# Kernel optimization log

Hardware: AMD Instinct MI355X
Metric: run time of the kernel (lower is better)

Reference implementation:

```python
import jax, jax.numpy as jnp
import numpy as np
import math

B, L, D_MODEL, D_K, H = 2, 1024, 1024, 1024, 16
HD = D_K // H  # 64, even
EPS = 1e-5


def setup_inputs() -> dict:
    key = jax.random.key(0)
    ks = jax.random.split(key, 16)
    s = 0.02
    inp = {
        'word_embed': jax.random.normal(ks[0], (B, L, D_MODEL), jnp.float32),
        'speaker_embed': jax.random.normal(ks[1], (B, L, D_MODEL), jnp.float32),
        'mask': jnp.broadcast_to(jnp.tril(jnp.ones((L, L), jnp.int32)), (B, L, L)),
        'qw_w': jax.random.normal(ks[2], (D_K, D_MODEL), jnp.float32) * s,
        'qw_b': jnp.zeros((D_K,), jnp.float32),
        'kw_w': jax.random.normal(ks[3], (D_K, D_MODEL), jnp.float32) * s,
        'kw_b': jnp.zeros((D_K,), jnp.float32),
        'qs_w': jax.random.normal(ks[4], (D_K, D_MODEL), jnp.float32) * s,
        'qs_b': jnp.zeros((D_K,), jnp.float32),
        'ks_w': jax.random.normal(ks[5], (D_K, D_MODEL), jnp.float32) * s,
        'ks_b': jnp.zeros((D_K,), jnp.float32),
        'v_w': jax.random.normal(ks[6], (D_K, D_MODEL), jnp.float32) * s,
        'v_b': jnp.zeros((D_K,), jnp.float32),
        'out_w': jax.random.normal(ks[7], (D_MODEL, D_K), jnp.float32) * s,
        'out_b': jnp.zeros((D_MODEL,), jnp.float32),
        'gamma': jnp.ones((HD,), jnp.float32),
        'beta': jnp.zeros((HD,), jnp.float32),
    }
    return inp


def _rotary_tables(seq_len, dim, dtype):
    pos = jnp.arange(seq_len, dtype=dtype)[:, None]  # [L,1]
    div = jnp.exp(jnp.arange(0, dim, 2, dtype=dtype) * (-math.log(10000.0) / dim))
    return jnp.sin(pos * div), jnp.cos(pos * div)  # each [L, dim//2]


def _rotary(x, sin, cos):
    # x: [B,H,L,HD]; NOTE: original concatenates halves (non-interleaved output)
    x1, x2 = x[..., 0::2], x[..., 1::2]
    return jnp.concatenate([x1 * cos - x2 * sin, x1 * sin + x2 * cos], axis=-1)


def _layernorm(x, gamma, beta):
    mu = jnp.mean(x, axis=-1, keepdims=True)
    var = jnp.mean(jnp.square(x - mu), axis=-1, keepdims=True)
    return (x - mu) * jax.lax.rsqrt(var + EPS) * gamma + beta


def _split(x):
    b, l, _ = x.shape
    return x.reshape(b, l, H, HD).transpose(0, 2, 1, 3)  # [B,H,L,HD]


def reference(word_embed, speaker_embed, mask, qw_w, qw_b, kw_w, kw_b,
              qs_w, qs_b, ks_w, ks_b, v_w, v_b, out_w, out_b, gamma, beta):
    proj = lambda x, w, b: jnp.einsum('bld,kd->blk', x, w) + b
    qw = _split(proj(word_embed, qw_w, qw_b))
    kw = _split(proj(word_embed, kw_w, kw_b))
    qs = _split(proj(speaker_embed, qs_w, qs_b))
    ks = _split(proj(speaker_embed, ks_w, ks_b))
    v = _split(proj(word_embed, v_w, v_b))

    sin, cos = _rotary_tables(word_embed.shape[1], HD, word_embed.dtype)
    ln = lambda x: _layernorm(_rotary(x, sin, cos), gamma, beta)
    qw, kw, qs, ks = ln(qw), ln(kw), ln(qs), ln(ks)

    scores = (jnp.einsum('bhqd,bhkd->bhqk', qw, kw)
              + jnp.einsum('bhqd,bhkd->bhqk', qs, ks)) / math.sqrt(2 * HD)
    scores = jnp.where(mask[:, None] == 0, -jnp.inf, scores)
    attn = jax.nn.softmax(scores, axis=-1)  # dropout is eval-mode no-op
    out = jnp.einsum('bhqk,bhkd->bhqd', attn, v)
    out = out.transpose(0, 2, 1, 3).reshape(out.shape[0], out.shape[2], D_K)
    out = jnp.einsum('blk,dk->bld', out, out_w) + out_b
    return (out, attn)
```

## Files before the change

kernel.cpp:

```cpp
#include <hip/hip_runtime.h>
#include <cstdint>
#include <cstddef>

typedef __bf16 bf16x8 __attribute__((ext_vector_type(8)));
typedef float  f32x4  __attribute__((ext_vector_type(4)));
typedef unsigned short ushort8_t __attribute__((ext_vector_type(8)));

__device__ __forceinline__ unsigned short f2bf(float f){
  unsigned u = __builtin_bit_cast(unsigned, f);
  u += 0x7fffu + ((u >> 16) & 1u);
  return (unsigned short)(u >> 16);
}
__device__ __forceinline__ float bf2f(unsigned short s){
  return __builtin_bit_cast(float, ((unsigned)s) << 16);
}

#define MFMA16(a,b,c) __builtin_amdgcn_mfma_f32_16x16x32_bf16((a),(b),(c),0,0,0)

__device__ __forceinline__ void gload16(const void* g, void* lds){
  __builtin_amdgcn_global_load_lds(
      (const __attribute__((address_space(1))) void*)g,
      (__attribute__((address_space(3))) void*)lds, 16, 0, 0);
}

#define E_XW    ((size_t)0)
#define E_XS    (E_XW    + (size_t)2048*1024)
#define E_WWORD (E_XS    + (size_t)2048*1024)
#define E_WSPK  (E_WWORD + (size_t)3072*1024)
#define E_WOUT  (E_WSPK  + (size_t)2048*1024)
#define E_PWORD (E_WOUT  + (size_t)1024*1024)
#define E_PSPK  (E_PWORD + (size_t)2048*3072)
#define E_VT    (E_PSPK  + (size_t)2048*2048)
#define E_CTX   (E_VT    + (size_t)2048*1024)
#define E_END   (E_CTX   + (size_t)2048*1024)

__global__ __launch_bounds__(256) void convert_all(
    const float* __restrict__ word, const float* __restrict__ spk,
    const float* __restrict__ qww,  const float* __restrict__ kww,
    const float* __restrict__ vw,   const float* __restrict__ qsw,
    const float* __restrict__ ksw,  const float* __restrict__ outw,
    const float* __restrict__ qwb,  const float* __restrict__ kwb,
    const float* __restrict__ vb,   const float* __restrict__ qsb,
    const float* __restrict__ ksb,
    unsigned short* __restrict__ wsb, float* __restrict__ FB)
{
  int idx = blockIdx.x*256 + threadIdx.x;
  if (idx < 32768){
    int pos = idx >> 5, i = idx & 31;
    float inv = expf((float)(2*i) * -0.14391157f);
    float ang = (float)pos * inv;
    float sv, cv; sincosf(ang, &sv, &cv);
    FB[5120 + idx]         = sv;
    FB[5120 + 32768 + idx] = cv;
  } else if (idx < 33792){
    int i = idx - 32768;
    FB[i] = qwb[i]; FB[1024+i] = kwb[i]; FB[2048+i] = vb[i];
    FB[3072+i] = qsb[i]; FB[3072+1024+i] = ksb[i];
  }

  const size_t total = 2621440;
  for (size_t c = (size_t)blockIdx.x*256 + threadIdx.x; c < total;
       c += (size_t)gridDim.x*256){
    const float* src; size_t dst; size_t i;
    if (c < 524288)       { src = word; dst = E_XW; i = c; }
    else if (c < 1048576) { src = spk;  dst = E_XS; i = c - 524288; }
    else {
      size_t t = c - 1048576; int seg = (int)(t >> 18); i = t & 262143;
      switch (seg){
        case 0:  src = qww; dst = E_WWORD;                      break;
        case 1:  src = kww; dst = E_WWORD + (size_t)1048576;    break;
        case 2:  src = vw;  dst = E_WWORD + (size_t)2097152;    break;
        case 3:  src = qsw; dst = E_WSPK;                       break;
        case 4:  src = ksw; dst = E_WSPK  + (size_t)1048576;    break;
        default: src = outw; dst = E_WOUT;                      break;
      }
    }
    float4 v = ((const float4*)src)[i];
    ushort4 o; o.x = f2bf(v.x); o.y = f2bf(v.y); o.z = f2bf(v.z); o.w = f2bf(v.w);
    ((ushort4*)(wsb + dst))[i] = o;
  }
}

template<int NF>
__device__ __forceinline__ void gemm_body(
    const unsigned short* __restrict__ A, const unsigned short* __restrict__ Bw,
    const float* __restrict__ bias, void* __restrict__ Cv,
    int N, int bid, int out_bf16,
    unsigned short* As, unsigned short* Bs)
{
  const int K = 1024;
  const int BN = NF*32;
  const int nbn = N / BN;
  const int bm = bid / nbn, bn = bid % nbn;
  const int tid = threadIdx.x;
  const int l = tid & 63, w = tid >> 6;
  const int wm = w >> 1, wn = w & 1;
  const int li = l & 15, lg = l >> 4;

  f32x4 acc[4][NF];
  #pragma unroll
  for (int a = 0; a < 4; a++)
    #pragma unroll
    for (int b = 0; b < NF; b++) acc[a][b] = (f32x4){0.f,0.f,0.f,0.f};

  const int colS = (l & 3) * 8;
  const size_t aBase = (size_t)(bm*128) * K;
  const size_t bBase = (size_t)(bn*BN) * K;

  for (int kt = 0; kt < K; kt += 32){
    #pragma unroll
    for (int j = 0; j < 2; j++){
      int row = (w*2 + j)*16 + (l >> 2);
      gload16(A + aBase + (size_t)row*K + kt + colS, &As[(size_t)(w*2+j)*512]);
    }
    if (NF == 4){
      #pragma unroll
      for (int j = 0; j < 2; j++){
        int row = (w*2 + j)*16 + (l >> 2);
        gload16(Bw + bBase + (size_t)row*K + kt + colS, &Bs[(size_t)(w*2+j)*512]);
      }
    } else {
      int row = w*16 + (l >> 2);
      gload16(Bw + bBase + (size_t)row*K + kt + colS, &Bs[(size_t)w*512]);
    }
    asm volatile("s_waitcnt vmcnt(0)" ::: "memory");
    __syncthreads();

    bf16x8 af[4], bfr[NF];
    const int ko = lg * 8;
    #pragma unroll
    for (int fm = 0; fm < 4; fm++)
      af[fm] = *(const bf16x8*)&As[(wm*64 + fm*16 + li)*32 + ko];
    #pragma unroll
    for (int fn = 0; fn < NF; fn++)
      bfr[fn] = *(const bf16x8*)&Bs[(wn*(NF*16) + fn*16 + li)*32 + ko];
    #pragma unroll
    for (int fm = 0; fm < 4; fm++)
      #pragma unroll
      for (int fn = 0; fn < NF; fn++)
        acc[fm][fn] = MFMA16(af[fm], bfr[fn], acc[fm][fn]);
    __syncthreads();
  }

  #pragma unroll
  for (int fm = 0; fm < 4; fm++){
    int m0 = bm*128 + wm*64 + fm*16 + lg*4;
    #pragma unroll
    for (int fn = 0; fn < NF; fn++){
      int n = bn*BN + wn*(NF*16) + fn*16 + li;
      float bv = bias[n];
      #pragma unroll
      for (int r = 0; r < 4; r++){
        float v = acc[fm][fn][r] + bv;
        if (out_bf16) ((unsigned short*)Cv)[(size_t)(m0+r)*N + n] = f2bf(v);
        else          ((float*)Cv)[(size_t)(m0+r)*N + n] = v;
      }
    }
  }
}

__global__ __launch_bounds__(256) void gemm_qkv(
    const unsigned short* __restrict__ XW, const unsigned short* __restrict__ WWORD,
    const unsigned short* __restrict__ XS, const unsigned short* __restrict__ WSPK,
    const float* __restrict__ FB,
    unsigned short* __restrict__ PWORD, unsigned short* __restrict__ PSPK)
{
  __shared__ unsigned short As[128*32];
  __shared__ unsigned short Bs[128*32];
  int raw = blockIdx.x;
  int bid = (raw & 7)*80 + (raw >> 3);
  if (bid < 384)
    gemm_body<4>(XW, WWORD, FB,        PWORD, 3072, bid,       1, As, Bs);
  else
    gemm_body<4>(XS, WSPK,  FB + 3072, PSPK,  2048, bid - 384, 1, As, Bs);
}

__global__ __launch_bounds__(256) void gemm_out(
    const unsigned short* __restrict__ CTX, const unsigned short* __restrict__ WOUT,
    const float* __restrict__ outb, float* __restrict__ outp)
{
  __shared__ unsigned short As[128*32];
  __shared__ unsigned short Bs[64*32];
  int raw = blockIdx.x;
  int bid = (raw & 7)*32 + (raw >> 3);
  gemm_body<2>(CTX, WOUT, outb, outp, 1024, bid, 0, As, Bs);
}

__global__ __launch_bounds__(256) void postproc(
    unsigned short* __restrict__ Pw, unsigned short* __restrict__ Ps,
    const float* __restrict__ gamma, const float* __restrict__ beta,
    const float* __restrict__ TS, const float* __restrict__ TC,
    unsigned short* __restrict__ VT)
{
  __shared__ float lds[2320];
  int bx = blockIdx.x;
  int t = threadIdx.x;
  if (bx < 4096){
    int sec = bx & 3, rp = bx >> 2;
    int half = t >> 7, c = t & 127;
    int row = rp*2 + half;
    int seg = c >> 3, j = c & 7;
    unsigned short* p;
    if      (sec == 0) p = Pw + (size_t)row*3072 +        seg*64;
    else if (sec == 1) p = Pw + (size_t)row*3072 + 1024 + seg*64;
    else if (sec == 2) p = Ps + (size_t)row*2048 +        seg*64;
    else               p = Ps + (size_t)row*2048 + 1024 + seg*64;
    int pos = row & 1023;
    int sl  = half*16 + seg;

    ushort8_t xv = *(const ushort8_t*)(p + j*8);
    float4 sv = *(const float4*)&TS[pos*32 + j*4];
    float4 cv = *(const float4*)&TC[pos*32 + j*4];
    float ss[4] = {sv.x, sv.y, sv.z, sv.w};
    float cc[4] = {cv.x, cv.y, cv.z, cv.w};
    float y1[4], y2[4];
    #pragma unroll
    for (int k = 0; k < 4; k++){
      float x0 = bf2f(xv[2*k]), x1 = bf2f(xv[2*k+1]);
      y1[k] = x0*cc[k] - x1*ss[k];
      y2[k] = x0*ss[k] + x1*cc[k];
    }
    *(float4*)&lds[sl*68 + j*4]      = (float4){y1[0], y1[1], y1[2], y1[3]};
    *(float4*)&lds[sl*68 + 32 + j*4] = (float4){y2[0], y2[1], y2[2], y2[3]};
    __syncthreads();

    float4 a0 = *(const float4*)&lds[sl*68 + j*8];
    float4 a1 = *(const float4*)&lds[sl*68 + j*8 + 4];
    float v[8] = {a0.x, a0.y, a0.z, a0.w, a1.x, a1.y, a1.z, a1.w};
    float s = 0.f;
    #pragma unroll
    for (int k = 0; k < 8; k++) s += v[k];
    #pragma unroll
    for (int o = 1; o < 8; o <<= 1) s += __shfl_xor(s, o);
    float mu = s * (1.f/64.f);
    float sq = 0.f;
    #pragma unroll
    for (int k = 0; k < 8; k++){ float d = v[k] - mu; sq += d*d; }
    #pragma unroll
    for (int o = 1; o < 8; o <<= 1) sq += __shfl_xor(sq, o);
    float rs = rsqrtf(sq * (1.f/64.f) + 1e-5f);
    float4 g0 = *(const float4*)&gamma[j*8], g1 = *(const float4*)&gamma[j*8+4];
    float4 b0 = *(const float4*)&beta[j*8],  b1 = *(const float4*)&beta[j*8+4];
    float gg[8] = {g0.x,g0.y,g0.z,g0.w,g1.x,g1.y,g1.z,g1.w};
    float bb[8] = {b0.x,b0.y,b0.z,b0.w,b1.x,b1.y,b1.z,b1.w};
    ushort8_t o8;
    #pragma unroll
    for (int k = 0; k < 8; k++) o8[k] = f2bf((v[k]-mu)*rs*gg[k] + bb[k]);
    *(ushort8_t*)(p + j*8) = o8;
  } else {
    unsigned short* tp = (unsigned short*)lds;
    int bid2 = bx - 4096;
    int bh = bid2 >> 4, lt = bid2 & 15;
    int b = bh >> 4, h = bh & 15;
    #pragma unroll
    for (int i = 0; i < 2; i++){
      int cc2 = t + i*256;
      int row = cc2 >> 3, co = (cc2 & 7)*8;
      const unsigned short* src = Pw + (size_t)(b*1024 + lt*64 + row)*3072 + 2048 + h*64 + co;
      *(uint4*)&tp[row*72 + co] = *(const uint4*)src;
    }
    __syncthreads();
    int d = t >> 2, jb = (t & 3)*16;
    unsigned short o[16];
    #pragma unroll
    for (int j = 0; j < 16; j++) o[j] = tp[(jb + j)*72 + d];
    unsigned short* dst = VT + ((size_t)bh*64 + d)*1024 + lt*64 + jb;
    *(uint4*)dst       = *(uint4*)&o[0];
    *(uint4*)(dst + 8) = *(uint4*)&o[8];
  }
}

__global__ __launch_bounds__(512) void attn_fused(
    const unsigned short* __restrict__ Pw, const unsigned short* __restrict__ Ps,
    const unsigned short* __restrict__ VTg,
    float* __restrict__ attn, unsigned short* __restrict__ Ctx)
{
  __shared__ unsigned short SL[36864];

  int bx = blockIdx.x;
  int b = bx >> 7, rem = bx & 127, h = rem >> 3, qq = rem & 7;
  int maxkt = 15 - qq;
  int tid = threadIdx.x;
  int w = tid >> 6, l = tid & 63;
  int g = w >> 2, wsub = w & 3;
  int qt = g ? maxkt : qq;
  int lg = l >> 4, li = l & 15;
  int q0 = qt*64 + wsub*16;
  int bh = b*16 + h;

  int srow = tid >> 3, scb = tid & 7;
  const unsigned short* gKW = Pw + (size_t)(b*1024)*3072 + 1024 + h*64;
  const unsigned short* gKS = Ps + (size_t)(b*1024)*2048 + 1024 + h*64;
  const unsigned short* gVT = VTg + (size_t)bh*64*1024;
  unsigned short* pt = SL + 27648 + w*1152;

  bf16x8 aqw[2], aqs[2];
  {
    int q = q0 + li;
    const unsigned short* pqw = Pw + (size_t)(b*1024 + q)*3072 + h*64 + lg*8;
    const unsigned short* pqs = Ps + (size_t)(b*1024 + q)*2048 + h*64 + lg*8;
    aqw[0] = *(const bf16x8*)pqw;  aqw[1] = *(const bf16x8*)(pqw + 32);
    aqs[0] = *(const bf16x8*)pqs;  aqs[1] = *(const bf16x8*)(pqs + 32);
  }
  const float rscale = 0.08838834764831845f;

  uint4 rkw, rks, rvt;

  float ps4[4] = {0.f, 0.f, 0.f, 0.f};
  rkw = *(const uint4*)(gKW + (size_t)srow*3072 + scb*8);
  rks = *(const uint4*)(gKS + (size_t)srow*2048 + scb*8);
  *(uint4*)(SL +        srow*72 + scb*8) = rkw;
  *(uint4*)(SL + 9216 + srow*72 + scb*8) = rks;

  for (int kt = 0; kt <= maxkt; ++kt){
    int buf = kt & 1;
    if (kt < maxkt){
      rkw = *(const uint4*)(gKW + (size_t)((kt+1)*64 + srow)*3072 + scb*8);
      rks = *(const uint4*)(gKS + (size_t)((kt+1)*64 + srow)*2048 + scb*8);
    }
    __syncthreads();
    if (kt <= qt){
      const unsigned short* KWt = SL +        buf*4608;
      const unsigned short* KSt = SL + 9216 + buf*4608;
      f32x4 s[4];
      #pragma unroll
      for (int fn = 0; fn < 4; fn++){
        s[fn] = (f32x4){0.f,0.f,0.f,0.f};
        int rr = (fn*16 + li)*72;
        bf16x8 k0 = *(const bf16x8*)(KWt + rr + lg*8);
        bf16x8 k1 = *(const bf16x8*)(KWt + rr + 32 + lg*8);
        bf16x8 k2 = *(const bf16x8*)(KSt + rr + lg*8);
        bf16x8 k3 = *(const bf16x8*)(KSt + rr + 32 + lg*8);
        s[fn] = MFMA16(aqw[0], k0, s[fn]);
        s[fn] = MFMA16(aqw[1], k1, s[fn]);
        s[fn] = MFMA16(aqs[0], k2, s[fn]);
        s[fn] = MFMA16(aqs[1], k3, s[fn]);
      }
      #pragma unroll
      for (int r = 0; r < 4; r++){
        int q = q0 + lg*4 + r;
        #pragma unroll
        for (int fn = 0; fn < 4; fn++){
          int k = kt*64 + fn*16 + li;
          float e = __expf(s[fn][r] * rscale);
          ps4[r] += (k <= q) ? e : 0.f;
        }
      }
    }
    if (kt < maxkt){
      int nb = buf ^ 1;
      *(uint4*)(SL +        nb*4608 + srow*72 + scb*8) = rkw;
      *(uint4*)(SL + 9216 + nb*4608 + srow*72 + scb*8) = rks;
    }
  }
  #pragma unroll
  for (int r = 0; r < 4; r++){
    #pragma unroll
    for (int o = 1; o < 16; o <<= 1) ps4[r] += __shfl_xor(ps4[r], o);
  }
  float rinv[4];
  #pragma unroll
  for (int r = 0; r < 4; r++) rinv[r] = 1.f / ps4[r];

  __syncthreads();
  rkw = *(const uint4*)(gKW + (size_t)srow*3072 + scb*8);
  rks = *(const uint4*)(gKS + (size_t)srow*2048 + scb*8);
  rvt = *(const uint4*)(gVT + (size_t)srow*1024 + scb*8);
  *(uint4*)(SL +         srow*72 + scb*8) = rkw;
  *(uint4*)(SL +  9216 + srow*72 + scb*8) = rks;
  *(uint4*)(SL + 18432 + srow*72 + scb*8) = rvt;

  f32x4 c[4];
  #pragma unroll
  for (int fn = 0; fn < 4; fn++) c[fn] = (f32x4){0.f,0.f,0.f,0.f};

  for (int kt = 0; kt < 16; ++kt){
    int buf = kt & 1;
    if (kt < maxkt){
      rkw = *(const uint4*)(gKW + (size_t)((kt+1)*64 + srow)*3072 + scb*8);
      rks = *(const uint4*)(gKS + (size_t)((kt+1)*64 + srow)*2048 + scb*8);
      rvt = *(const uint4*)(gVT + (size_t)srow*1024 + (kt+1)*64 + scb*8);
    }
    __syncthreads();
    float* abase = attn + ((size_t)bh*1024 + q0 + li)*1024 + kt*64;
    if (kt <= qt){
      const unsigned short* KWt = SL +         buf*4608;
      const unsigned short* KSt = SL +  9216 + buf*4608;
      const unsigned short* VTt = SL + 18432 + buf*4608;
      f32x4 s[4];
      #pragma unroll
      for (int fn = 0; fn < 4; fn++){
        s[fn] = (f32x4){0.f,0.f,0.f,0.f};
        int rr = (fn*16 + li)*72;
        bf16x8 k0 = *(const bf16x8*)(KWt + rr + lg*8);
        bf16x8 k1 = *(const bf16x8*)(KWt + rr + 32 + lg*8);
        bf16x8 k2 = *(const bf16x8*)(KSt + rr + lg*8);
        bf16x8 k3 = *(const bf16x8*)(KSt + rr + 32 + lg*8);
        s[fn] = MFMA16(aqw[0], k0, s[fn]);
        s[fn] = MFMA16(aqw[1], k1, s[fn]);
        s[fn] = MFMA16(aqs[0], k2, s[fn]);
        s[fn] = MFMA16(aqs[1], k3, s[fn]);
      }
      #pragma unroll
      for (int fn = 0; fn < 4; fn++){
        #pragma unroll
        for (int r = 0; r < 4; r++){
          int k = kt*64 + fn*16 + li;
          int q = q0 + lg*4 + r;
          float pp = (k <= q) ? __expf(s[fn][r] * rscale) * rinv[r] : 0.f;
          pt[(lg*4 + r)*72 + fn*16 + li] = f2bf(pp);
        }
      }
      asm volatile("s_waitcnt lgkmcnt(0)" ::: "memory");
      __builtin_amdgcn_sched_barrier(0);
      bf16x8 af0 = *(const bf16x8*)(pt + li*72 + lg*8);
      bf16x8 af1 = *(const bf16x8*)(pt + li*72 + 32 + lg*8);
      ushort8_t u0 = __builtin_bit_cast(ushort8_t, af0);
      ushort8_t u1 = __builtin_bit_cast(ushort8_t, af1);
      *(float4*)(abase + lg*8)          = (float4){bf2f(u0[0]),bf2f(u0[1]),bf2f(u0[2]),bf2f(u0[3])};
      *(float4*)(abase + lg*8 + 4)      = (float4){bf2f(u0[4]),bf2f(u0[5]),bf2f(u0[6]),bf2f(u0[7])};
      *(float4*)(abase + 32 + lg*8)     = (float4){bf2f(u1[0]),bf2f(u1[1]),bf2f(u1[2]),bf2f(u1[3])};
      *(float4*)(abase + 32 + lg*8 + 4) = (float4){bf2f(u1[4]),bf2f(u1[5]),bf2f(u1[6]),bf2f(u1[7])};
      #pragma unroll
      for (int fn = 0; fn < 4; fn++){
        int rr = (fn*16 + li)*72;
        bf16x8 v0 = *(const bf16x8*)(VTt + rr + lg*8);
        bf16x8 v1 = *(const bf16x8*)(VTt + rr + 32 + lg*8);
        c[fn] = MFMA16(af0, v0, c[fn]);
        c[fn] = MFMA16(af1, v1, c[fn]);
      }
    } else {
      float4 z = {0.f, 0.f, 0.f, 0.f};
      *(float4*)(abase + lg*8)          = z;
      *(float4*)(abase + lg*8 + 4)      = z;
      *(float4*)(abase + 32 + lg*8)     = z;
      *(float4*)(abase + 32 + lg*8 + 4) = z;
    }
    if (kt < maxkt){
      int nb = buf ^ 1;
      *(uint4*)(SL +         nb*4608 + srow*72 + scb*8) = rkw;
      *(uint4*)(SL +  9216 + nb*4608 + srow*72 + scb*8) = rks;
      *(uint4*)(SL + 18432 + nb*4608 + srow*72 + scb*8) = rvt;
    }
  }

  #pragma unroll
  for (int fn = 0; fn < 4; fn++){
    #pragma unroll
    for (int r = 0; r < 4; r++){
      int q = q0 + lg*4 + r;
      int d = fn*16 + li;
      Ctx[(size_t)(b*1024 + q)*1024 + h*64 + d] = f2bf(c[fn][r]);
    }
  }
}

extern "C" void kernel_launch(void* const* d_in, const int* in_sizes, int n_in,
                              void* d_out, int out_size, void* d_ws, size_t ws_size,
                              hipStream_t stream)
{
  (void)in_sizes; (void)n_in; (void)out_size; (void)ws_size;
  const float* word = (const float*)d_in[0];
  const float* spk  = (const float*)d_in[1];
  const float* qww  = (const float*)d_in[3];
  const float* qwb  = (const float*)d_in[4];
  const float* kww  = (const float*)d_in[5];
  const float* kwb  = (const float*)d_in[6];
  const float* qsw  = (const float*)d_in[7];
  const float* qsb  = (const float*)d_in[8];
  const float* ksw  = (const float*)d_in[9];
  const float* ksb  = (const float*)d_in[10];
  const float* vw   = (const float*)d_in[11];
  const float* vb   = (const float*)d_in[12];
  const float* outw = (const float*)d_in[13];
  const float* outb = (const float*)d_in[14];
  const float* gamma= (const float*)d_in[15];
  const float* beta = (const float*)d_in[16];

  unsigned short* U = (unsigned short*)d_ws;
  unsigned short* XW    = U + E_XW;
  unsigned short* XS    = U + E_XS;
  unsigned short* WWORD = U + E_WWORD;
  unsigned short* WSPK  = U + E_WSPK;
  unsigned short* WOUT  = U + E_WOUT;
  unsigned short* PWORD = U + E_PWORD;
  unsigned short* PSPK  = U + E_PSPK;
  unsigned short* VT    = U + E_VT;
  unsigned short* CTX   = U + E_CTX;
  float* FB = (float*)(U + E_END);
  float* TS = FB + 5120;
  float* TC = TS + 32768;

  float* outp = (float*)d_out;
  float* attn = outp + (size_t)2*1024*1024;

  convert_all<<<4096, 256, 0, stream>>>(word, spk, qww, kww, vw, qsw, ksw, outw,
                                        qwb, kwb, vb, qsb, ksb, U, FB);
  gemm_qkv<<<640, 256, 0, stream>>>(XW, WWORD, XS, WSPK, FB, PWORD, PSPK);
  postproc<<<4608, 256, 0, stream>>>(PWORD, PSPK, gamma, beta, TS, TC, VT);
  attn_fused<<<256, 512, 0, stream>>>(PWORD, PSPK, VT, attn, CTX);
  gemm_out<<<256, 256, 0, stream>>>(CTX, WOUT, outb, outp);
}
```

Before: 117.8 us.

## Split paired-tile attention blocks into one query tile per block with swizzled order

```diff
diff --git a/kernel.cpp b/kernel.cpp
--- a/kernel.cpp
+++ b/kernel.cpp
@@ -270,25 +270,24 @@
   }
 }
 
-__global__ __launch_bounds__(512) void attn_fused(
+__global__ __launch_bounds__(256) void attn_fused(
     const unsigned short* __restrict__ Pw, const unsigned short* __restrict__ Ps,
     const unsigned short* __restrict__ VTg,
     float* __restrict__ attn, unsigned short* __restrict__ Ctx)
 {
-  __shared__ unsigned short SL[36864];
-
-  int bx = blockIdx.x;
-  int b = bx >> 7, rem = bx & 127, h = rem >> 3, qq = rem & 7;
-  int maxkt = 15 - qq;
+  __shared__ unsigned short SL[32256];
+
+  int raw = blockIdx.x;
+  int bx  = (raw & 7)*64 + (raw >> 3);
+  int b = bx >> 8, rem = bx & 255, h = rem >> 4;
+  int qt = 15 - (rem & 15);
   int tid = threadIdx.x;
   int w = tid >> 6, l = tid & 63;
-  int g = w >> 2, wsub = w & 3;
-  int qt = g ? maxkt : qq;
   int lg = l >> 4, li = l & 15;
-  int q0 = qt*64 + wsub*16;
+  int q0 = qt*64 + w*16;
   int bh = b*16 + h;
 
-  int srow = tid >> 3, scb = tid & 7;
+  int sr = tid >> 3, sc = tid & 7;
   const unsigned short* gKW = Pw + (size_t)(b*1024)*3072 + 1024 + h*64;
   const unsigned short* gKS = Ps + (size_t)(b*1024)*2048 + 1024 + h*64;
   const unsigned short* gVT = VTg + (size_t)bh*64*1024;
@@ -304,23 +303,29 @@
   }
   const float rscale = 0.08838834764831845f;
 
-  uint4 rkw, rks, rvt;
+  uint4 ka0, ka1, kb0, kb1, va0, va1;
 
   float ps4[4] = {0.f, 0.f, 0.f, 0.f};
-  rkw = *(const uint4*)(gKW + (size_t)srow*3072 + scb*8);
-  rks = *(const uint4*)(gKS + (size_t)srow*2048 + scb*8);
-  *(uint4*)(SL +        srow*72 + scb*8) = rkw;
-  *(uint4*)(SL + 9216 + srow*72 + scb*8) = rks;
-
-  for (int kt = 0; kt <= maxkt; ++kt){
+  ka0 = *(const uint4*)(gKW + (size_t)sr*3072 + sc*8);
+  ka1 = *(const uint4*)(gKW + (size_t)(sr+32)*3072 + sc*8);
+  kb0 = *(const uint4*)(gKS + (size_t)sr*2048 + sc*8);
+  kb1 = *(const uint4*)(gKS + (size_t)(sr+32)*2048 + sc*8);
+  *(uint4*)(SL + sr*72 + sc*8) = ka0;
+  *(uint4*)(SL + (sr+32)*72 + sc*8) = ka1;
+  *(uint4*)(SL + 9216 + sr*72 + sc*8) = kb0;
+  *(uint4*)(SL + 9216 + (sr+32)*72 + sc*8) = kb1;
+
+  for (int kt = 0; kt <= qt; ++kt){
     int buf = kt & 1;
-    if (kt < maxkt){
-      rkw = *(const uint4*)(gKW + (size_t)((kt+1)*64 + srow)*3072 + scb*8);
-      rks = *(const uint4*)(gKS + (size_t)((kt+1)*64 + srow)*2048 + scb*8);
+    if (kt < qt){
+      ka0 = *(const uint4*)(gKW + (size_t)((kt+1)*64 + sr)*3072 + sc*8);
+      ka1 = *(const uint4*)(gKW + (size_t)((kt+1)*64 + sr+32)*3072 + sc*8);
+      kb0 = *(const uint4*)(gKS + (size_t)((kt+1)*64 + sr)*2048 + sc*8);
+      kb1 = *(const uint4*)(gKS + (size_t)((kt+1)*64 + sr+32)*2048 + sc*8);
     }
     __syncthreads();
-    if (kt <= qt){
-      const unsigned short* KWt = SL +        buf*4608;
+    {
+      const unsigned short* KWt = SL + buf*4608;
       const unsigned short* KSt = SL + 9216 + buf*4608;
       f32x4 s[4];
       #pragma unroll
@@ -347,10 +352,12 @@
         }
       }
     }
-    if (kt < maxkt){
+    if (kt < qt){
       int nb = buf ^ 1;
-      *(uint4*)(SL +        nb*4608 + srow*72 + scb*8) = rkw;
-      *(uint4*)(SL + 9216 + nb*4608 + srow*72 + scb*8) = rks;
+      *(uint4*)(SL + nb*4608 + sr*72 + sc*8) = ka0;
+      *(uint4*)(SL + nb*4608 + (sr+32)*72 + sc*8) = ka1;
+      *(uint4*)(SL + 9216 + nb*4608 + sr*72 + sc*8) = kb0;
+      *(uint4*)(SL + 9216 + nb*4608 + (sr+32)*72 + sc*8) = kb1;
     }
   }
   #pragma unroll
@@ -363,29 +370,38 @@
   for (int r = 0; r < 4; r++) rinv[r] = 1.f / ps4[r];
 
   __syncthreads();
-  rkw = *(const uint4*)(gKW + (size_t)srow*3072 + scb*8);
-  rks = *(const uint4*)(gKS + (size_t)srow*2048 + scb*8);
-  rvt = *(const uint4*)(gVT + (size_t)srow*1024 + scb*8);
-  *(uint4*)(SL +         srow*72 + scb*8) = rkw;
-  *(uint4*)(SL +  9216 + srow*72 + scb*8) = rks;
-  *(uint4*)(SL + 18432 + srow*72 + scb*8) = rvt;
+  ka0 = *(const uint4*)(gKW + (size_t)sr*3072 + sc*8);
+  ka1 = *(const uint4*)(gKW + (size_t)(sr+32)*3072 + sc*8);
+  kb0 = *(const uint4*)(gKS + (size_t)sr*2048 + sc*8);
+  kb1 = *(const uint4*)(gKS + (size_t)(sr+32)*2048 + sc*8);
+  va0 = *(const uint4*)(gVT + (size_t)sr*1024 + sc*8);
+  va1 = *(const uint4*)(gVT + (size_t)(sr+32)*1024 + sc*8);
+  *(uint4*)(SL + sr*72 + sc*8) = ka0;
+  *(uint4*)(SL + (sr+32)*72 + sc*8) = ka1;
+  *(uint4*)(SL + 9216 + sr*72 + sc*8) = kb0;
+  *(uint4*)(SL + 9216 + (sr+32)*72 + sc*8) = kb1;
+  *(uint4*)(SL + 18432 + sr*72 + sc*8) = va0;
+  *(uint4*)(SL + 18432 + (sr+32)*72 + sc*8) = va1;
 
   f32x4 c[4];
   #pragma unroll
   for (int fn = 0; fn < 4; fn++) c[fn] = (f32x4){0.f,0.f,0.f,0.f};
 
-  for (int kt = 0; kt < 16; ++kt){
+  for (int kt = 0; kt <= qt; ++kt){
     int buf = kt & 1;
-    if (kt < maxkt){
-      rkw = *(const uint4*)(gKW + (size_t)((kt+1)*64 + srow)*3072 + scb*8);
-      rks = *(const uint4*)(gKS + (size_t)((kt+1)*64 + srow)*2048 + scb*8);
-      rvt = *(const uint4*)(gVT + (size_t)srow*1024 + (kt+1)*64 + scb*8);
+    if (kt < qt){
+      ka0 = *(const uint4*)(gKW + (size_t)((kt+1)*64 + sr)*3072 + sc*8);
+      ka1 = *(const uint4*)(gKW + (size_t)((kt+1)*64 + sr+32)*3072 + sc*8);
+      kb0 = *(const uint4*)(gKS + (size_t)((kt+1)*64 + sr)*2048 + sc*8);
+      kb1 = *(const uint4*)(gKS + (size_t)((kt+1)*64 + sr+32)*2048 + sc*8);
+      va0 = *(const uint4*)(gVT + (size_t)sr*1024 + (kt+1)*64 + sc*8);
+      va1 = *(const uint4*)(gVT + (size_t)(sr+32)*1024 + (kt+1)*64 + sc*8);
     }
     __syncthreads();
     float* abase = attn + ((size_t)bh*1024 + q0 + li)*1024 + kt*64;
-    if (kt <= qt){
-      const unsigned short* KWt = SL +         buf*4608;
-      const unsigned short* KSt = SL +  9216 + buf*4608;
+    {
+      const unsigned short* KWt = SL + buf*4608;
+      const unsigned short* KSt = SL + 9216 + buf*4608;
       const unsigned short* VTt = SL + 18432 + buf*4608;
       f32x4 s[4];
       #pragma unroll
@@ -429,19 +445,25 @@
         c[fn] = MFMA16(af0, v0, c[fn]);
         c[fn] = MFMA16(af1, v1, c[fn]);
       }
-    } else {
-      float4 z = {0.f, 0.f, 0.f, 0.f};
-      *(float4*)(abase + lg*8)          = z;
-      *(float4*)(abase + lg*8 + 4)      = z;
-      *(float4*)(abase + 32 + lg*8)     = z;
-      *(float4*)(abase + 32 + lg*8 + 4) = z;
-    }
-    if (kt < maxkt){
+    }
+    if (kt < qt){
       int nb = buf ^ 1;
-      *(uint4*)(SL +         nb*4608 + srow*72 + scb*8) = rkw;
-      *(uint4*)(SL +  9216 + nb*4608 + srow*72 + scb*8) = rks;
-      *(uint4*)(SL + 18432 + nb*4608 + srow*72 + scb*8) = rvt;
-    }
+      *(uint4*)(SL + nb*4608 + sr*72 + sc*8) = ka0;
+      *(uint4*)(SL + nb*4608 + (sr+32)*72 + sc*8) = ka1;
+      *(uint4*)(SL + 9216 + nb*4608 + sr*72 + sc*8) = kb0;
+      *(uint4*)(SL + 9216 + nb*4608 + (sr+32)*72 + sc*8) = kb1;
+      *(uint4*)(SL + 18432 + nb*4608 + sr*72 + sc*8) = va0;
+      *(uint4*)(SL + 18432 + nb*4608 + (sr+32)*72 + sc*8) = va1;
+    }
+  }
+
+  for (int kt = qt + 1; kt < 16; ++kt){
+    float* abase = attn + ((size_t)bh*1024 + q0 + li)*1024 + kt*64;
+    float4 z = {0.f, 0.f, 0.f, 0.f};
+    *(float4*)(abase + lg*8)          = z;
+    *(float4*)(abase + lg*8 + 4)      = z;
+    *(float4*)(abase + 32 + lg*8)     = z;
+    *(float4*)(abase + 32 + lg*8 + 4) = z;
   }
 
   #pragma unroll
@@ -498,6 +520,6 @@
                                         qwb, kwb, vb, qsb, ksb, U, FB);
   gemm_qkv<<<640, 256, 0, stream>>>(XW, WWORD, XS, WSPK, FB, PWORD, PSPK);
   postproc<<<4608, 256, 0, stream>>>(PWORD, PSPK, gamma, beta, TS, TC, VT);
-  attn_fused<<<256, 512, 0, stream>>>(PWORD, PSPK, VT, attn, CTX);
+  attn_fused<<<512, 256, 0, stream>>>(PWORD, PSPK, VT, attn, CTX);
   gemm_out<<<256, 256, 0, stream>>>(CTX, WOUT, outb, outp);
 }
```

Measured after the change: 121.1 us. 1.03x slower.
